# Optimization experiments

Hardware: AMD Instinct MI355X
Metric: run time of the kernel (lower is better)

The kernel has to match this reference:

```python
import jax, jax.numpy as jnp
import numpy as np

N = 50000          # nb_nodes
DEG = 32           # avg degree -> every node has DEG outgoing edges (rows covered)
E = N * DEG        # 1,600,000 edges
F_IN = 512
F_OUT = 256


def setup_inputs() -> dict:
    key = jax.random.key(0)
    k = jax.random.split(key, 8)
    x = jax.random.normal(k[0], (1, N, F_IN), dtype=jnp.float32)
    W = jax.random.normal(k[1], (F_IN, F_OUT), dtype=jnp.float32) * 0.05
    a1_w = jax.random.normal(k[2], (F_OUT, 1), dtype=jnp.float32) * 0.05
    a1_b = jnp.zeros((1,), jnp.float32)
    a2_w = jax.random.normal(k[3], (F_OUT, 1), dtype=jnp.float32) * 0.05
    a2_b = jnp.zeros((1,), jnp.float32)
    bias_out = jnp.zeros((F_OUT,), jnp.float32)
    # edge list: each node has exactly DEG neighbors (rows sorted, all rows present)
    edge_row = jnp.repeat(jnp.arange(N, dtype=jnp.int32), DEG)
    edge_col = jax.random.randint(k[4], (E,), 0, N, dtype=jnp.int32)
    bias_vals = jnp.ones((E,), jnp.float32)  # SparseTensor values of bias_mat
    return {"x": x, "W": W, "a1_w": a1_w, "a1_b": a1_b, "a2_w": a2_w,
            "a2_b": a2_b, "bias_out": bias_out, "bias_vals": bias_vals,
            "edge_row": edge_row, "edge_col": edge_col}


def reference(x, W, a1_w, a1_b, a2_w, a2_b, bias_out, bias_vals, edge_row, edge_col):
    # conv1d(k=1, no bias): per-node linear projection. x: [1, N, F_IN]
    seq = jnp.einsum('nf,fo->no', x[0], W)                 # [N, F_OUT]
    f1 = (seq @ a1_w + a1_b)[:, 0]                         # [N]
    f2 = (seq @ a2_w + a2_b)[:, 0]                         # [N]
    # sparse_add(bias_mat*f1_row, bias_mat^T-style*f2_col) -> per-edge logits
    e = bias_vals * f1[edge_row] + bias_vals * f2[edge_col]  # [E]
    e = jax.nn.leaky_relu(e, negative_slope=0.2)
    # sparse_softmax: softmax over nonzero entries of each row
    row_max = jax.ops.segment_max(e, edge_row, num_segments=N)
    row_max = jnp.where(jnp.isfinite(row_max), row_max, 0.0)
    ee = jnp.exp(e - row_max[edge_row])
    denom = jax.ops.segment_sum(ee, edge_row, num_segments=N)
    coefs = ee / jnp.maximum(denom[edge_row], 1e-30)        # [E]
    # SpMM: out[i] = sum_j coefs[ij] * seq[j]
    vals = jax.ops.segment_sum(coefs[:, None] * seq[edge_col], edge_row,
                               num_segments=N)             # [N, F_OUT]
    ret = jax.nn.elu(vals + bias_out)[None]                # [1, N, F_OUT]
    return ret
```

## Files before the change

### kernel.cpp

```cpp
#include <hip/hip_runtime.h>
#include <stdint.h>

#define N_NODES 50000
#define DEG 32
#define FIN 512
#define FOUT 256

typedef __attribute__((ext_vector_type(4))) float f32x4;
typedef __attribute__((ext_vector_type(8))) short short8;

__device__ __forceinline__ unsigned short f2bf(float f) {
    union { float f; unsigned int u; } v; v.f = f;
    unsigned int u = v.u;
    return (unsigned short)((u + 0x7FFFu + ((u >> 16) & 1u)) >> 16);
}

__device__ __forceinline__ void gll16(const void* g, void* l) {
    __builtin_amdgcn_global_load_lds(
        (const __attribute__((address_space(1))) unsigned int*)g,
        (__attribute__((address_space(3))) unsigned int*)(uintptr_t)l,
        16, 0, 0);
}

__global__ void k_wt2(const float* __restrict__ W, unsigned short* __restrict__ Wt2) {
    int idx = blockIdx.x * 256 + threadIdx.x;
    int e    = idx & 7;
    int j    = (idx >> 3) & 63;
    int frag = (idx >> 9) & 31;
    int t    = idx >> 14;
    int n = (frag >> 1) * 16 + (j & 15);
    int k = t * 64 + (frag & 1) * 32 + (j >> 4) * 8 + e;
    Wt2[idx] = f2bf(W[k * FOUT + n]);
}

#define GBM 64
#define GBK 64

__global__ __launch_bounds__(512, 2)
void k_gemm(const float* __restrict__ x, const unsigned short* __restrict__ Wt2,
            const float* __restrict__ a1w, const float* __restrict__ a1b,
            const float* __restrict__ a2w, const float* __restrict__ a2b,
            float* __restrict__ f1, float* __restrict__ f2,
            float* __restrict__ scale, unsigned int* __restrict__ seq8) {
    __shared__ unsigned short As[2][8 * 512];
    __shared__ unsigned short Bs[2][32 * 512];

    const int tid  = threadIdx.x;
    const int lane = tid & 63;
    const int w    = tid >> 6;
    const int row0 = blockIdx.x * GBM;
    const int fr   = lane & 15;
    const int fq   = lane >> 4;
    const int mg = w >> 2, ng = w & 3;
    const int n0 = ng * 64;

    const int r_ = lane >> 3, q_ = lane & 7;
    int arow = row0 + w * 8 + r_;
    if (arow >= N_NODES) arow = N_NODES - 1;
    const float* aptr = x + (size_t)arow * FIN + q_ * 8;
    const int rowlow = (w & 1) * 8 + r_;
    const int awoff = ((((w >> 1) * 2 + (q_ >> 2)) << 9)
                       + ((((q_ & 3) << 4) | (rowlow ^ (q_ & 3))) << 3));

    const unsigned short* bsrc0 = Wt2 + ((w * 4 + 0) << 9) + lane * 8;
    const unsigned short* bsrc1 = Wt2 + ((w * 4 + 1) << 9) + lane * 8;
    const unsigned short* bsrc2 = Wt2 + ((w * 4 + 2) << 9) + lane * 8;
    const unsigned short* bsrc3 = Wt2 + ((w * 4 + 3) << 9) + lane * 8;
    const int bo0 = ((w * 4 + 0) << 9) + lane * 8;
    const int bo1 = ((w * 4 + 1) << 9) + lane * 8;
    const int bo2 = ((w * 4 + 2) << 9) + lane * 8;
    const int bo3 = ((w * 4 + 3) << 9) + lane * 8;

    const int mf0 = mg * 2;
    const int nc0 = ng * 4;
    const int axr = ((fq << 4) | (fr ^ fq)) << 3;

    f32x4 acc[2][4];
    f32x4 zero4 = {0.f, 0.f, 0.f, 0.f};
#pragma unroll
    for (int i = 0; i < 2; i++)
#pragma unroll
        for (int j = 0; j < 4; j++) acc[i][j] = zero4;

    float4 sa0, sa1;
#define STAGE_A_LOAD(T) \
    sa0 = *(const float4*)(aptr + (T) * GBK); \
    sa1 = *(const float4*)(aptr + (T) * GBK + 4);
#define STAGE_A_WRITE(BUF) \
    { short8 pk; \
      pk[0] = (short)f2bf(sa0.x); pk[1] = (short)f2bf(sa0.y); \
      pk[2] = (short)f2bf(sa0.z); pk[3] = (short)f2bf(sa0.w); \
      pk[4] = (short)f2bf(sa1.x); pk[5] = (short)f2bf(sa1.y); \
      pk[6] = (short)f2bf(sa1.z); pk[7] = (short)f2bf(sa1.w); \
      *(short8*)(void*)&As[BUF][awoff] = pk; }

    gll16(bsrc0, &Bs[0][bo0]);
    gll16(bsrc1, &Bs[0][bo1]);
    gll16(bsrc2, &Bs[0][bo2]);
    gll16(bsrc3, &Bs[0][bo3]);
    STAGE_A_LOAD(0)
    STAGE_A_WRITE(0)
    __syncthreads();

    for (int t = 0; t < 8; ++t) {
        const int rb = t & 1, wb = rb ^ 1;
        if (t < 7) {
            const int ko = (t + 1) * 16384;
            gll16(bsrc0 + ko, &Bs[wb][bo0]);
            gll16(bsrc1 + ko, &Bs[wb][bo1]);
            gll16(bsrc2 + ko, &Bs[wb][bo2]);
            gll16(bsrc3 + ko, &Bs[wb][bo3]);
            STAGE_A_LOAD(t + 1)
        }
#pragma unroll
        for (int s = 0; s < 2; ++s) {
            short8 a0 = *(const short8*)(const void*)&As[rb][(((mf0 + 0) * 2 + s) << 9) + axr];
            short8 a1 = *(const short8*)(const void*)&As[rb][(((mf0 + 1) * 2 + s) << 9) + axr];
            short8 b0 = *(const short8*)(const void*)&Bs[rb][(((nc0 + 0) * 2 + s) << 9) + lane * 8];
            short8 b1 = *(const short8*)(const void*)&Bs[rb][(((nc0 + 1) * 2 + s) << 9) + lane * 8];
            short8 b2 = *(const short8*)(const void*)&Bs[rb][(((nc0 + 2) * 2 + s) << 9) + lane * 8];
            short8 b3 = *(const short8*)(const void*)&Bs[rb][(((nc0 + 3) * 2 + s) << 9) + lane * 8];
            acc[0][0] = __builtin_amdgcn_mfma_f32_16x16x32_bf16(a0, b0, acc[0][0], 0, 0, 0);
            acc[0][1] = __builtin_amdgcn_mfma_f32_16x16x32_bf16(a0, b1, acc[0][1], 0, 0, 0);
            acc[0][2] = __builtin_amdgcn_mfma_f32_16x16x32_bf16(a0, b2, acc[0][2], 0, 0, 0);
            acc[0][3] = __builtin_amdgcn_mfma_f32_16x16x32_bf16(a0, b3, acc[0][3], 0, 0, 0);
            acc[1][0] = __builtin_amdgcn_mfma_f32_16x16x32_bf16(a1, b0, acc[1][0], 0, 0, 0);
            acc[1][1] = __builtin_amdgcn_mfma_f32_16x16x32_bf16(a1, b1, acc[1][1], 0, 0, 0);
            acc[1][2] = __builtin_amdgcn_mfma_f32_16x16x32_bf16(a1, b2, acc[1][2], 0, 0, 0);
            acc[1][3] = __builtin_amdgcn_mfma_f32_16x16x32_bf16(a1, b3, acc[1][3], 0, 0, 0);
        }
        if (t < 7) {
            STAGE_A_WRITE(wb)
            __syncthreads();
        }
    }

    __syncthreads();
    float* f1p_l  = (float*)(void*)As;
    float* f2p_l  = f1p_l + 256;
    float* am_l   = f2p_l + 256;
    float* finv_l = am_l + 256;

    const float w10 = a1w[n0 + fr],      w11 = a1w[n0 + 16 + fr];
    const float w12 = a1w[n0 + 32 + fr], w13 = a1w[n0 + 48 + fr];
    const float w20 = a2w[n0 + fr],      w21 = a2w[n0 + 16 + fr];
    const float w22 = a2w[n0 + 32 + fr], w23 = a2w[n0 + 48 + fr];

#pragma unroll
    for (int mi = 0; mi < 2; mi++) {
#pragma unroll
        for (int r = 0; r < 4; r++) {
            float c0 = acc[mi][0][r], c1 = acc[mi][1][r];
            float c2 = acc[mi][2][r], c3 = acc[mi][3][r];
            float s1 = c0 * w10 + c1 * w11 + c2 * w12 + c3 * w13;
            float s2 = c0 * w20 + c1 * w21 + c2 * w22 + c3 * w23;
            float am = fmaxf(fmaxf(fabsf(c0), fabsf(c1)),
                             fmaxf(fabsf(c2), fabsf(c3)));
#pragma unroll
            for (int off = 1; off < 16; off <<= 1) {
                s1 += __shfl_xor(s1, off, 64);
                s2 += __shfl_xor(s2, off, 64);
                am = fmaxf(am, __shfl_xor(am, off, 64));
            }
            if (fr == 0) {
                int rowb = mg * 32 + mi * 16 + fq * 4 + r;
                f1p_l[rowb * 4 + ng] = s1;
                f2p_l[rowb * 4 + ng] = s2;
                am_l[rowb * 4 + ng]  = am;
            }
        }
    }
    __syncthreads();

    if (tid < 64) {
        float4 p1 = *(const float4*)&f1p_l[tid * 4];
        float4 p2 = *(const float4*)&f2p_l[tid * 4];
        float4 pm = *(const float4*)&am_l[tid * 4];
        float s1 = p1.x + p1.y + p1.z + p1.w + a1b[0];
        float s2 = p2.x + p2.y + p2.z + p2.w + a2b[0];
        float am = fmaxf(fmaxf(pm.x, pm.y), fmaxf(pm.z, pm.w));
        am = fmaxf(am, 1e-8f);
        int grow = row0 + tid;
        if (grow < N_NODES) {
            f1[grow] = s1;
            f2[grow] = s2;
            scale[grow] = am * (1.0f / 127.0f);
        }
        finv_l[tid] = 127.0f / am;
    }
    __syncthreads();

#pragma unroll
    for (int mi = 0; mi < 2; mi++) {
#pragma unroll
        for (int r = 0; r < 4; r++) {
            int rowb = mg * 32 + mi * 16 + fq * 4 + r;
            int grow = row0 + rowb;
            float inv = finv_l[rowb];
            int q0 = ((int)rintf(acc[mi][0][r] * inv)) & 255;
            int q1 = ((int)rintf(acc[mi][1][r] * inv)) & 255;
            int q2 = ((int)rintf(acc[mi][2][r] * inv)) & 255;
            int q3 = ((int)rintf(acc[mi][3][r] * inv)) & 255;
            unsigned int pk = ((unsigned int)q0 | ((unsigned int)q1 << 8) |
                               ((unsigned int)q2 << 16) | ((unsigned int)q3 << 24))
                              ^ 0x80808080u;
            if (grow < N_NODES)
                seq8[(size_t)grow * 64 + ng * 16 + fr] = pk;
        }
    }
}

#define LOADS(J) \
    int          c##J = __shfl(col,  (J), 64); \
    float        w##J = __shfl(coef, (J), 64); \
    unsigned int v##J = *(const unsigned int*)(const void*)(sp + (size_t)c##J * 64);

#define ACCUM(J) \
    a0 += w##J * (float)( v##J        & 0xffu); \
    a1 += w##J * (float)((v##J >>  8) & 0xffu); \
    a2 += w##J * (float)((v##J >> 16) & 0xffu); \
    a3 += w##J * (float)( v##J >> 24       );

__global__ __launch_bounds__(256, 4)
void k_attn(const unsigned int* __restrict__ seq8, const float* __restrict__ scale,
            const float* __restrict__ f1, const float* __restrict__ f2,
            const float* __restrict__ bias_vals,
            const int* __restrict__ edge_col,
            const float* __restrict__ bias_out,
            float* __restrict__ out) {
    const int lane = threadIdx.x & 63;
    const int node = (blockIdx.x * 256 + threadIdx.x) >> 6;

    float e = -1e30f;
    int col = 0;
    float sc = 0.f;
    if (lane < 32) {
        int eidx = node * DEG + lane;
        col = edge_col[eidx];
        sc  = scale[col];
        float bv = bias_vals[eidx];
        e = bv * f1[node] + bv * f2[col];
        e = (e >= 0.f) ? e : 0.2f * e;
    }
    float m = e;
#pragma unroll
    for (int off = 16; off; off >>= 1) m = fmaxf(m, __shfl_xor(m, off, 32));
    float p = __expf(e - m);
    float s = p;
#pragma unroll
    for (int off = 16; off; off >>= 1) s += __shfl_xor(s, off, 32);
    float coef = p * __builtin_amdgcn_rcpf(s) * sc;

    float ws = coef;
#pragma unroll
    for (int off = 16; off; off >>= 1) ws += __shfl_xor(ws, off, 32);
    float corr = 128.0f * __shfl(ws, 0, 64);

    const unsigned int* sp = seq8 + lane;
    float a0 = 0.f, a1 = 0.f, a2 = 0.f, a3 = 0.f;
    {
        LOADS(0) LOADS(1) LOADS(2) LOADS(3) LOADS(4) LOADS(5) LOADS(6) LOADS(7)
        ACCUM(0) ACCUM(1) ACCUM(2) ACCUM(3) ACCUM(4) ACCUM(5) ACCUM(6) ACCUM(7)
    }
    {
        LOADS(8) LOADS(9) LOADS(10) LOADS(11) LOADS(12) LOADS(13) LOADS(14) LOADS(15)
        ACCUM(8) ACCUM(9) ACCUM(10) ACCUM(11) ACCUM(12) ACCUM(13) ACCUM(14) ACCUM(15)
    }
    {
        LOADS(16) LOADS(17) LOADS(18) LOADS(19) LOADS(20) LOADS(21) LOADS(22) LOADS(23)
        ACCUM(16) ACCUM(17) ACCUM(18) ACCUM(19) ACCUM(20) ACCUM(21) ACCUM(22) ACCUM(23)
    }
    {
        LOADS(24) LOADS(25) LOADS(26) LOADS(27) LOADS(28) LOADS(29) LOADS(30) LOADS(31)
        ACCUM(24) ACCUM(25) ACCUM(26) ACCUM(27) ACCUM(28) ACCUM(29) ACCUM(30) ACCUM(31)
    }

    const int fb = (lane >> 4) * 64 + (lane & 15);
    float b0 = bias_out[fb], b1 = bias_out[fb + 16];
    float b2 = bias_out[fb + 32], b3 = bias_out[fb + 48];
    float r0 = a0 - corr + b0, r1 = a1 - corr + b1;
    float r2 = a2 - corr + b2, r3 = a3 - corr + b3;
    r0 = (r0 > 0.f) ? r0 : (__expf(r0) - 1.0f);
    r1 = (r1 > 0.f) ? r1 : (__expf(r1) - 1.0f);
    r2 = (r2 > 0.f) ? r2 : (__expf(r2) - 1.0f);
    r3 = (r3 > 0.f) ? r3 : (__expf(r3) - 1.0f);
    float* op = out + (size_t)node * FOUT + fb;
    op[0]  = r0;
    op[16] = r1;
    op[32] = r2;
    op[48] = r3;
}

extern "C" void kernel_launch(void* const* d_in, const int* in_sizes, int n_in,
                              void* d_out, int out_size, void* d_ws, size_t ws_size,
                              hipStream_t stream) {
    const float* x         = (const float*)d_in[0];
    const float* W         = (const float*)d_in[1];
    const float* a1w       = (const float*)d_in[2];
    const float* a1b       = (const float*)d_in[3];
    const float* a2w       = (const float*)d_in[4];
    const float* a2b       = (const float*)d_in[5];
    const float* bias_out  = (const float*)d_in[6];
    const float* bias_vals = (const float*)d_in[7];
    const int* edge_col    = (const int*)d_in[9];
    float* out = (float*)d_out;

    char* ws = (char*)d_ws;
    unsigned short* Wt2 = (unsigned short*)ws;
    float* f1    = (float*)(ws + 262144);
    float* f2    = (float*)(ws + 262144 + 200064);
    float* scale = (float*)(ws + 262144 + 2 * 200064);
    unsigned int* seq8 = (unsigned int*)(ws + 262144 + 3 * 200064);

    hipLaunchKernelGGL(k_wt2, dim3(512), dim3(256), 0, stream, W, Wt2);
    hipLaunchKernelGGL(k_gemm, dim3((N_NODES + GBM - 1) / GBM), dim3(512), 0, stream,
                       x, Wt2, a1w, a1b, a2w, a2b, f1, f2, scale, seq8);
    hipLaunchKernelGGL(k_attn, dim3(N_NODES / 4), dim3(256), 0, stream,
                       seq8, scale, f1, f2, bias_vals, edge_col,
                       bias_out, out);
}
```

Measured before the change: 101.0 us.

## Gather neighbor rows via global_load_lds with staged vmcnt waits in attention kernel

Each wave now issues all 32 neighbor-row gathers as 4-byte global_load_lds into a per-wave LDS buffer, then consumes them in groups of eight behind progressively looser vmcnt waits. This keeps all 32 gathers in flight without holding them in registers, which lowers VGPR pressure; launch bounds are raised to 5 blocks per SM to use the freed registers for occupancy. The cost is 32 KB of LDS per block, which may itself limit occupancy. It also relies on hand-placed waitcnt and sched_barrier ordering being correct for LDS-direct loads.

```diff
diff --git a/kernel.cpp b/kernel.cpp
--- a/kernel.cpp
+++ b/kernel.cpp
@@ -20,6 +20,12 @@
         (const __attribute__((address_space(1))) unsigned int*)g,
         (__attribute__((address_space(3))) unsigned int*)(uintptr_t)l,
         16, 0, 0);
+}
+__device__ __forceinline__ void gll4(const void* g, void* l) {
+    __builtin_amdgcn_global_load_lds(
+        (const __attribute__((address_space(1))) unsigned int*)g,
+        (__attribute__((address_space(3))) unsigned int*)(uintptr_t)l,
+        4, 0, 0);
 }
 
 __global__ void k_wt2(const float* __restrict__ W, unsigned short* __restrict__ Wt2) {
@@ -210,25 +216,24 @@
     }
 }
 
-#define LOADS(J) \
-    int          c##J = __shfl(col,  (J), 64); \
-    float        w##J = __shfl(coef, (J), 64); \
-    unsigned int v##J = *(const unsigned int*)(const void*)(sp + (size_t)c##J * 64);
-
-#define ACCUM(J) \
-    a0 += w##J * (float)( v##J        & 0xffu); \
-    a1 += w##J * (float)((v##J >>  8) & 0xffu); \
-    a2 += w##J * (float)((v##J >> 16) & 0xffu); \
-    a3 += w##J * (float)( v##J >> 24       );
-
-__global__ __launch_bounds__(256, 4)
+#define CONS(J) \
+    { float c = __shfl(coef, (J), 64); \
+      unsigned int u = gbuf[wv][(J)][lane]; \
+      a0 += c * (float)( u        & 0xffu); \
+      a1 += c * (float)((u >>  8) & 0xffu); \
+      a2 += c * (float)((u >> 16) & 0xffu); \
+      a3 += c * (float)( u >> 24       ); }
+
+__global__ __launch_bounds__(256, 5)
 void k_attn(const unsigned int* __restrict__ seq8, const float* __restrict__ scale,
             const float* __restrict__ f1, const float* __restrict__ f2,
             const float* __restrict__ bias_vals,
             const int* __restrict__ edge_col,
             const float* __restrict__ bias_out,
             float* __restrict__ out) {
+    __shared__ unsigned int gbuf[4][32][64];
     const int lane = threadIdx.x & 63;
+    const int wv   = threadIdx.x >> 6;
     const int node = (blockIdx.x * 256 + threadIdx.x) >> 6;
 
     float e = -1e30f;
@@ -256,24 +261,28 @@
     for (int off = 16; off; off >>= 1) ws += __shfl_xor(ws, off, 32);
     float corr = 128.0f * __shfl(ws, 0, 64);
 
+    asm volatile("s_waitcnt vmcnt(0)" ::: "memory");
     const unsigned int* sp = seq8 + lane;
+#pragma unroll
+    for (int j = 0; j < 32; ++j) {
+        int cj = __shfl(col, j, 64);
+        gll4(sp + (size_t)cj * 64, &gbuf[wv][j][0]);
+    }
+
     float a0 = 0.f, a1 = 0.f, a2 = 0.f, a3 = 0.f;
-    {
-        LOADS(0) LOADS(1) LOADS(2) LOADS(3) LOADS(4) LOADS(5) LOADS(6) LOADS(7)
-        ACCUM(0) ACCUM(1) ACCUM(2) ACCUM(3) ACCUM(4) ACCUM(5) ACCUM(6) ACCUM(7)
-    }
-    {
-        LOADS(8) LOADS(9) LOADS(10) LOADS(11) LOADS(12) LOADS(13) LOADS(14) LOADS(15)
-        ACCUM(8) ACCUM(9) ACCUM(10) ACCUM(11) ACCUM(12) ACCUM(13) ACCUM(14) ACCUM(15)
-    }
-    {
-        LOADS(16) LOADS(17) LOADS(18) LOADS(19) LOADS(20) LOADS(21) LOADS(22) LOADS(23)
-        ACCUM(16) ACCUM(17) ACCUM(18) ACCUM(19) ACCUM(20) ACCUM(21) ACCUM(22) ACCUM(23)
-    }
-    {
-        LOADS(24) LOADS(25) LOADS(26) LOADS(27) LOADS(28) LOADS(29) LOADS(30) LOADS(31)
-        ACCUM(24) ACCUM(25) ACCUM(26) ACCUM(27) ACCUM(28) ACCUM(29) ACCUM(30) ACCUM(31)
-    }
+
+    asm volatile("s_waitcnt vmcnt(24)" ::: "memory");
+    __builtin_amdgcn_sched_barrier(0);
+    CONS(0)  CONS(1)  CONS(2)  CONS(3)  CONS(4)  CONS(5)  CONS(6)  CONS(7)
+    asm volatile("s_waitcnt vmcnt(16)" ::: "memory");
+    __builtin_amdgcn_sched_barrier(0);
+    CONS(8)  CONS(9)  CONS(10) CONS(11) CONS(12) CONS(13) CONS(14) CONS(15)
+    asm volatile("s_waitcnt vmcnt(8)" ::: "memory");
+    __builtin_amdgcn_sched_barrier(0);
+    CONS(16) CONS(17) CONS(18) CONS(19) CONS(20) CONS(21) CONS(22) CONS(23)
+    asm volatile("s_waitcnt vmcnt(0)" ::: "memory");
+    __builtin_amdgcn_sched_barrier(0);
+    CONS(24) CONS(25) CONS(26) CONS(27) CONS(28) CONS(29) CONS(30) CONS(31)
 
     const int fb = (lane >> 4) * 64 + (lane & 15);
     float b0 = bias_out[fb], b1 = bias_out[fb + 16];
```

After: 114.8 us. 1.14x slower.

## Split int8 feature table into four planes and gather each in separate passes

Applied to the files above, without the earlier changes.

The GEMM now writes the quantized seq8 table as four planes of 64 features (3.2 MB each) instead of row-interleaved. Attention coefficients are computed once in a separate kernel and stored to workspace. Four gather passes then each read one plane, so each pass's random neighbor gathers hit a working set that fits better in cache. Each lane handles 8 edges for one 16-word slice and reduces across lane groups with shuffles. The cost is extra launches, rereading edge_col and coefficients four times, and an added coefficient buffer round-trip.

```diff
diff --git a/kernel.cpp b/kernel.cpp
--- a/kernel.cpp
+++ b/kernel.cpp
@@ -205,29 +205,17 @@
                                ((unsigned int)q2 << 16) | ((unsigned int)q3 << 24))
                               ^ 0x80808080u;
             if (grow < N_NODES)
-                seq8[(size_t)grow * 64 + ng * 16 + fr] = pk;
-        }
-    }
-}
-
-#define LOADS(J) \
-    int          c##J = __shfl(col,  (J), 64); \
-    float        w##J = __shfl(coef, (J), 64); \
-    unsigned int v##J = *(const unsigned int*)(const void*)(sp + (size_t)c##J * 64);
-
-#define ACCUM(J) \
-    a0 += w##J * (float)( v##J        & 0xffu); \
-    a1 += w##J * (float)((v##J >>  8) & 0xffu); \
-    a2 += w##J * (float)((v##J >> 16) & 0xffu); \
-    a3 += w##J * (float)( v##J >> 24       );
-
-__global__ __launch_bounds__(256, 4)
-void k_attn(const unsigned int* __restrict__ seq8, const float* __restrict__ scale,
+                seq8[((size_t)(ng * N_NODES + grow) << 4) + fr] = pk;
+        }
+    }
+}
+
+__global__ __launch_bounds__(256, 8)
+void k_coef(const float* __restrict__ scale,
             const float* __restrict__ f1, const float* __restrict__ f2,
             const float* __restrict__ bias_vals,
             const int* __restrict__ edge_col,
-            const float* __restrict__ bias_out,
-            float* __restrict__ out) {
+            float* __restrict__ coefb, float* __restrict__ corrb) {
     const int lane = threadIdx.x & 63;
     const int node = (blockIdx.x * 256 + threadIdx.x) >> 6;
 
@@ -250,45 +238,59 @@
 #pragma unroll
     for (int off = 16; off; off >>= 1) s += __shfl_xor(s, off, 32);
     float coef = p * __builtin_amdgcn_rcpf(s) * sc;
-
     float ws = coef;
 #pragma unroll
     for (int off = 16; off; off >>= 1) ws += __shfl_xor(ws, off, 32);
-    float corr = 128.0f * __shfl(ws, 0, 64);
-
-    const unsigned int* sp = seq8 + lane;
+    if (lane < 32) coefb[node * 32 + lane] = coef;
+    if (lane == 0) corrb[node] = 128.0f * ws;
+}
+
+#define PLOAD(R, S) \
+    { int cj##S = __shfl(colv, (R) * 4 + g, 64); \
+      c##S = __shfl(cfv, (R) * 4 + g, 64); \
+      u##S = plane[(size_t)cj##S * 16 + w]; }
+
+#define PACC(S) \
+    a0 += c##S * (float)( u##S        & 0xffu); \
+    a1 += c##S * (float)((u##S >>  8) & 0xffu); \
+    a2 += c##S * (float)((u##S >> 16) & 0xffu); \
+    a3 += c##S * (float)( u##S >> 24       );
+
+__global__ __launch_bounds__(256, 8)
+void k_pass(const unsigned int* __restrict__ plane,
+            const float* __restrict__ coefb, const float* __restrict__ corrb,
+            const int* __restrict__ edge_col,
+            const float* __restrict__ bias_out,
+            float* __restrict__ out, int p) {
+    const int lane = threadIdx.x & 63;
+    const int node = (blockIdx.x * 256 + threadIdx.x) >> 6;
+
+    int colv = 0;
+    float cfv = 0.f;
+    if (lane < 32) {
+        colv = edge_col[node * 32 + lane];
+        cfv  = coefb[node * 32 + lane];
+    }
+    const int g = lane >> 4, w = lane & 15;
+
     float a0 = 0.f, a1 = 0.f, a2 = 0.f, a3 = 0.f;
-    {
-        LOADS(0) LOADS(1) LOADS(2) LOADS(3) LOADS(4) LOADS(5) LOADS(6) LOADS(7)
-        ACCUM(0) ACCUM(1) ACCUM(2) ACCUM(3) ACCUM(4) ACCUM(5) ACCUM(6) ACCUM(7)
-    }
-    {
-        LOADS(8) LOADS(9) LOADS(10) LOADS(11) LOADS(12) LOADS(13) LOADS(14) LOADS(15)
-        ACCUM(8) ACCUM(9) ACCUM(10) ACCUM(11) ACCUM(12) ACCUM(13) ACCUM(14) ACCUM(15)
-    }
-    {
-        LOADS(16) LOADS(17) LOADS(18) LOADS(19) LOADS(20) LOADS(21) LOADS(22) LOADS(23)
-        ACCUM(16) ACCUM(17) ACCUM(18) ACCUM(19) ACCUM(20) ACCUM(21) ACCUM(22) ACCUM(23)
-    }
-    {
-        LOADS(24) LOADS(25) LOADS(26) LOADS(27) LOADS(28) LOADS(29) LOADS(30) LOADS(31)
-        ACCUM(24) ACCUM(25) ACCUM(26) ACCUM(27) ACCUM(28) ACCUM(29) ACCUM(30) ACCUM(31)
-    }
-
-    const int fb = (lane >> 4) * 64 + (lane & 15);
-    float b0 = bias_out[fb], b1 = bias_out[fb + 16];
-    float b2 = bias_out[fb + 32], b3 = bias_out[fb + 48];
-    float r0 = a0 - corr + b0, r1 = a1 - corr + b1;
-    float r2 = a2 - corr + b2, r3 = a3 - corr + b3;
-    r0 = (r0 > 0.f) ? r0 : (__expf(r0) - 1.0f);
-    r1 = (r1 > 0.f) ? r1 : (__expf(r1) - 1.0f);
-    r2 = (r2 > 0.f) ? r2 : (__expf(r2) - 1.0f);
-    r3 = (r3 > 0.f) ? r3 : (__expf(r3) - 1.0f);
-    float* op = out + (size_t)node * FOUT + fb;
-    op[0]  = r0;
-    op[16] = r1;
-    op[32] = r2;
-    op[48] = r3;
+    unsigned int u0, u1, u2, u3, u4, u5, u6, u7;
+    float c0, c1, c2, c3, c4, c5, c6, c7;
+
+    PLOAD(0, 0) PLOAD(1, 1) PLOAD(2, 2) PLOAD(3, 3)
+    PLOAD(4, 4) PLOAD(5, 5) PLOAD(6, 6) PLOAD(7, 7)
+    PACC(0) PACC(1) PACC(2) PACC(3) PACC(4) PACC(5) PACC(6) PACC(7)
+
+    a0 += __shfl_xor(a0, 16, 64); a1 += __shfl_xor(a1, 16, 64);
+    a2 += __shfl_xor(a2, 16, 64); a3 += __shfl_xor(a3, 16, 64);
+    a0 += __shfl_xor(a0, 32, 64); a1 += __shfl_xor(a1, 32, 64);
+    a2 += __shfl_xor(a2, 32, 64); a3 += __shfl_xor(a3, 32, 64);
+
+    float v = (g == 0) ? a0 : (g == 1) ? a1 : (g == 2) ? a2 : a3;
+    const int fb = p * 64 + lane;
+    float r = v - corrb[node] + bias_out[fb];
+    r = (r > 0.f) ? r : (__expf(r) - 1.0f);
+    out[(size_t)node * FOUT + fb] = r;
 }
 
 extern "C" void kernel_launch(void* const* d_in, const int* in_sizes, int n_in,
@@ -310,12 +312,19 @@
     float* f1    = (float*)(ws + 262144);
     float* f2    = (float*)(ws + 262144 + 200064);
     float* scale = (float*)(ws + 262144 + 2 * 200064);
-    unsigned int* seq8 = (unsigned int*)(ws + 262144 + 3 * 200064);
+    float* corrb = (float*)(ws + 262144 + 3 * 200064);
+    unsigned int* seq8 = (unsigned int*)(ws + 262144 + 4 * 200064);
+    float* coefb = (float*)(ws + 262144 + 4 * 200064 + 12800000);
 
     hipLaunchKernelGGL(k_wt2, dim3(512), dim3(256), 0, stream, W, Wt2);
     hipLaunchKernelGGL(k_gemm, dim3((N_NODES + GBM - 1) / GBM), dim3(512), 0, stream,
                        x, Wt2, a1w, a1b, a2w, a2b, f1, f2, scale, seq8);
-    hipLaunchKernelGGL(k_attn, dim3(N_NODES / 4), dim3(256), 0, stream,
-                       seq8, scale, f1, f2, bias_vals, edge_col,
-                       bias_out, out);
-}
+    hipLaunchKernelGGL(k_coef, dim3(N_NODES / 4), dim3(256), 0, stream,
+                       scale, f1, f2, bias_vals, edge_col, coefb, corrb);
+#pragma unroll
+    for (int p = 0; p < 4; ++p) {
+        hipLaunchKernelGGL(k_pass, dim3(N_NODES / 4), dim3(256), 0, stream,
+                           seq8 + (size_t)p * N_NODES * 16, coefb, corrb,
+                           edge_col, bias_out, out, p);
+    }
+}
```

Result: slower. 127.2 us (+26.0%).

## Halve B LDS staging to K=32 sub-steps and raise occupancy to six blocks

Applied to the files above, without the earlier changes.

Splits each 64-wide K tile of the GEMM into two 32-wide sub-steps, so the B stage buffer in LDS shrinks to half its size. Launch bounds rise from 2 to 6 blocks per CU. A tiles are still staged every 64 K while B is double-buffered per 32 K step. This is meant to raise occupancy and hide latency, at the cost of twice as many block barriers, tighter register limits and possible spills.

```diff
diff --git a/kernel.cpp b/kernel.cpp
--- a/kernel.cpp
+++ b/kernel.cpp
@@ -34,16 +34,15 @@
 }
 
 #define GBM 64
-#define GBK 64
-
-__global__ __launch_bounds__(512, 2)
+
+__global__ __launch_bounds__(512, 6)
 void k_gemm(const float* __restrict__ x, const unsigned short* __restrict__ Wt2,
             const float* __restrict__ a1w, const float* __restrict__ a1b,
             const float* __restrict__ a2w, const float* __restrict__ a2b,
             float* __restrict__ f1, float* __restrict__ f2,
             float* __restrict__ scale, unsigned int* __restrict__ seq8) {
     __shared__ unsigned short As[2][8 * 512];
-    __shared__ unsigned short Bs[2][32 * 512];
+    __shared__ unsigned short Bs[2][16 * 512];
 
     const int tid  = threadIdx.x;
     const int lane = tid & 63;
@@ -62,14 +61,8 @@
     const int awoff = ((((w >> 1) * 2 + (q_ >> 2)) << 9)
                        + ((((q_ & 3) << 4) | (rowlow ^ (q_ & 3))) << 3));
 
-    const unsigned short* bsrc0 = Wt2 + ((w * 4 + 0) << 9) + lane * 8;
-    const unsigned short* bsrc1 = Wt2 + ((w * 4 + 1) << 9) + lane * 8;
-    const unsigned short* bsrc2 = Wt2 + ((w * 4 + 2) << 9) + lane * 8;
-    const unsigned short* bsrc3 = Wt2 + ((w * 4 + 3) << 9) + lane * 8;
-    const int bo0 = ((w * 4 + 0) << 9) + lane * 8;
-    const int bo1 = ((w * 4 + 1) << 9) + lane * 8;
-    const int bo2 = ((w * 4 + 2) << 9) + lane * 8;
-    const int bo3 = ((w * 4 + 3) << 9) + lane * 8;
+    const int bo0 = ((2 * w + 0) << 9) + lane * 8;
+    const int bo1 = ((2 * w + 1) << 9) + lane * 8;
 
     const int mf0 = mg * 2;
     const int nc0 = ng * 4;
@@ -84,8 +77,8 @@
 
     float4 sa0, sa1;
 #define STAGE_A_LOAD(T) \
-    sa0 = *(const float4*)(aptr + (T) * GBK); \
-    sa1 = *(const float4*)(aptr + (T) * GBK + 4);
+    sa0 = *(const float4*)(aptr + (T) * 64); \
+    sa1 = *(const float4*)(aptr + (T) * 64 + 4);
 #define STAGE_A_WRITE(BUF) \
     { short8 pk; \
       pk[0] = (short)f2bf(sa0.x); pk[1] = (short)f2bf(sa0.y); \
@@ -94,32 +87,30 @@
       pk[6] = (short)f2bf(sa1.z); pk[7] = (short)f2bf(sa1.w); \
       *(short8*)(void*)&As[BUF][awoff] = pk; }
 
-    gll16(bsrc0, &Bs[0][bo0]);
-    gll16(bsrc1, &Bs[0][bo1]);
-    gll16(bsrc2, &Bs[0][bo2]);
-    gll16(bsrc3, &Bs[0][bo3]);
+#define STAGE_B(T, BUF) \
+    { const unsigned short* bs = Wt2 + ((T) >> 1) * 16384 \
+                                 + ((4 * w + ((T) & 1)) << 9) + lane * 8; \
+      gll16(bs,        &Bs[BUF][bo0]); \
+      gll16(bs + 1024, &Bs[BUF][bo1]); }
+
+    STAGE_B(0, 0)
     STAGE_A_LOAD(0)
     STAGE_A_WRITE(0)
     __syncthreads();
 
-    for (int t = 0; t < 8; ++t) {
-        const int rb = t & 1, wb = rb ^ 1;
-        if (t < 7) {
-            const int ko = (t + 1) * 16384;
-            gll16(bsrc0 + ko, &Bs[wb][bo0]);
-            gll16(bsrc1 + ko, &Bs[wb][bo1]);
-            gll16(bsrc2 + ko, &Bs[wb][bo2]);
-            gll16(bsrc3 + ko, &Bs[wb][bo3]);
-            STAGE_A_LOAD(t + 1)
-        }
-#pragma unroll
-        for (int s = 0; s < 2; ++s) {
-            short8 a0 = *(const short8*)(const void*)&As[rb][(((mf0 + 0) * 2 + s) << 9) + axr];
-            short8 a1 = *(const short8*)(const void*)&As[rb][(((mf0 + 1) * 2 + s) << 9) + axr];
-            short8 b0 = *(const short8*)(const void*)&Bs[rb][(((nc0 + 0) * 2 + s) << 9) + lane * 8];
-            short8 b1 = *(const short8*)(const void*)&Bs[rb][(((nc0 + 1) * 2 + s) << 9) + lane * 8];
-            short8 b2 = *(const short8*)(const void*)&Bs[rb][(((nc0 + 2) * 2 + s) << 9) + lane * 8];
-            short8 b3 = *(const short8*)(const void*)&Bs[rb][(((nc0 + 3) * 2 + s) << 9) + lane * 8];
+    for (int t = 0; t < 16; ++t) {
+        const int bb = t & 1;
+        const int tb = (t >> 1) & 1;
+        if (t < 15) STAGE_B(t + 1, bb ^ 1)
+        if ((t & 1) == 0 && t < 14) { STAGE_A_LOAD((t >> 1) + 1) }
+        {
+            const int s = t & 1;
+            short8 a0 = *(const short8*)(const void*)&As[tb][(((mf0 + 0) * 2 + s) << 9) + axr];
+            short8 a1 = *(const short8*)(const void*)&As[tb][(((mf0 + 1) * 2 + s) << 9) + axr];
+            short8 b0 = *(const short8*)(const void*)&Bs[bb][((nc0 + 0) << 9) + lane * 8];
+            short8 b1 = *(const short8*)(const void*)&Bs[bb][((nc0 + 1) << 9) + lane * 8];
+            short8 b2 = *(const short8*)(const void*)&Bs[bb][((nc0 + 2) << 9) + lane * 8];
+            short8 b3 = *(const short8*)(const void*)&Bs[bb][((nc0 + 3) << 9) + lane * 8];
             acc[0][0] = __builtin_amdgcn_mfma_f32_16x16x32_bf16(a0, b0, acc[0][0], 0, 0, 0);
             acc[0][1] = __builtin_amdgcn_mfma_f32_16x16x32_bf16(a0, b1, acc[0][1], 0, 0, 0);
             acc[0][2] = __builtin_amdgcn_mfma_f32_16x16x32_bf16(a0, b2, acc[0][2], 0, 0, 0);
@@ -129,10 +120,8 @@
             acc[1][2] = __builtin_amdgcn_mfma_f32_16x16x32_bf16(a1, b2, acc[1][2], 0, 0, 0);
             acc[1][3] = __builtin_amdgcn_mfma_f32_16x16x32_bf16(a1, b3, acc[1][3], 0, 0, 0);
         }
-        if (t < 7) {
-            STAGE_A_WRITE(wb)
-            __syncthreads();
-        }
+        if ((t & 1) == 1 && t < 15) { STAGE_A_WRITE(((t >> 1) + 1) & 1) }
+        if (t < 15) __syncthreads();
     }
 
     __syncthreads();
```

Result: no change. 102.0 us (+1.0%).
